# Kernel tuning notes

Hardware: AMD Instinct MI355X
Metric: run time of the kernel (lower is better)

Reference implementation:

```python
import jax, jax.numpy as jnp
import numpy as np

D_MODEL = 512
NUM_HEADS = 8
D_K = D_MODEL // NUM_HEADS


def setup_inputs() -> dict:
    key = jax.random.key(0)
    k0, k1, k2, k3, k4 = jax.random.split(key, 5)
    s = 1.0 / np.sqrt(D_MODEL)
    return {
        "x": jax.random.normal(k0, (2, 4096, D_MODEL), dtype=jnp.float32),
        "W_q": jax.random.normal(k1, (D_MODEL, D_MODEL), dtype=jnp.float32) * s,
        "W_k": jax.random.normal(k2, (D_MODEL, D_MODEL), dtype=jnp.float32) * s,
        "W_v": jax.random.normal(k3, (D_MODEL, D_MODEL), dtype=jnp.float32) * s,
        "W_o": jax.random.normal(k4, (D_MODEL, D_MODEL), dtype=jnp.float32) * s,
    }


def reference(x, W_q, W_k, W_v, W_o):
    B, S, _ = x.shape
    # project and split heads: (B, H, S, d_k)
    def split(t):
        return t.reshape(B, S, NUM_HEADS, D_K).transpose(0, 2, 1, 3)
    Q = split(x @ W_q)
    K = split(x @ W_k)
    V = split(x @ W_v)
    scale = jnp.sqrt(jnp.asarray(D_K, dtype=x.dtype))
    logits = jnp.einsum('bhqd,bhkd->bhqk', Q, K) / scale
    attn = jax.nn.softmax(logits, axis=-1)  # dropout is identity at inference
    out = jnp.einsum('bhqk,bhkd->bhqd', attn, V)
    concat = out.transpose(0, 2, 1, 3).reshape(B, S, D_MODEL)
    return concat @ W_o
```

## Files before the change

kernel.cpp:

```cpp
#include <hip/hip_runtime.h>
#include <hip/hip_bf16.h>


#define DMODEL 512
#define SEQ    4096
#define NTOK   8192
#define LDQK   1024

using f32x4 = __attribute__((ext_vector_type(4))) float;
using s16x8 = __attribute__((ext_vector_type(8))) short;
using u16x8 = __attribute__((ext_vector_type(8))) unsigned short;

static __device__ __forceinline__ unsigned short f2bf(float f) {
  union { float f; unsigned u; } v; v.f = f;
  unsigned r = v.u + 0x7fff + ((v.u >> 16) & 1);
  return (unsigned short)(r >> 16);
}

static __device__ __forceinline__ unsigned pack_bf2(float lo, float hi) {
  __hip_bfloat162 t = __float22bfloat162_rn(make_float2(lo, hi));
  union { __hip_bfloat162 b; unsigned u; } c; c.b = t; return c.u;
}

static __device__ __forceinline__ void gll16(const void* g, void* l) {
  __builtin_amdgcn_global_load_lds(
      (const __attribute__((address_space(1))) unsigned int*)g,
      (__attribute__((address_space(3))) unsigned int*)l, 16, 0, 0);
}

__global__ void prep_kernel(const float* __restrict__ x,
                            const float* __restrict__ Wq,
                            const float* __restrict__ Wk,
                            const float* __restrict__ Wv,
                            const float* __restrict__ Wo,
                            unsigned short* __restrict__ xb,
                            unsigned short* __restrict__ Wall, float c2) {
  __shared__ float T[64][65];
  const int bx = blockIdx.x;
  if (bx < 1024) {
    for (int i = bx * 256 + threadIdx.x; i < NTOK * DMODEL / 4; i += 262144) {
      float4 v = ((const float4*)x)[i];
      ushort4 o;
      o.x = f2bf(v.x); o.y = f2bf(v.y); o.z = f2bf(v.z); o.w = f2bf(v.w);
      ((ushort4*)xb)[i] = o;
    }
    return;
  }
  const int t = bx - 1024;
  const int y = t >> 6, sub = t & 63;
  const float* W = (y == 0) ? Wq : (y == 1) ? Wk : (y == 2) ? Wv : Wo;
  const float scale = (y == 0) ? c2 : 1.0f;
  const int tk = (sub & 7) * 64;
  const int tn = (sub >> 3) * 64;
  const int r  = threadIdx.x >> 2;
  const int cq = threadIdx.x & 3;
#pragma unroll
  for (int i = 0; i < 4; ++i) {
    int c = (cq + 4 * i) * 4;
    float4 v = *(const float4*)&W[(size_t)(tk + r) * 512 + tn + c];
    T[r][c + 0] = v.x * scale; T[r][c + 1] = v.y * scale;
    T[r][c + 2] = v.z * scale; T[r][c + 3] = v.w * scale;
  }
  __syncthreads();
  const int n  = threadIdx.x >> 2;
  const int k0 = (threadIdx.x & 3) * 16;
#pragma unroll
  for (int j4 = 0; j4 < 4; ++j4) {
    ushort4 o;
    o.x = f2bf(T[k0 + j4 * 4 + 0][n]);
    o.y = f2bf(T[k0 + j4 * 4 + 1][n]);
    o.z = f2bf(T[k0 + j4 * 4 + 2][n]);
    o.w = f2bf(T[k0 + j4 * 4 + 3][n]);
    *(ushort4*)&Wall[(size_t)y * 262144 + (size_t)(tn + n) * 512 + tk + k0 + j4 * 4] = o;
  }
}

__global__ __launch_bounds__(256, 3) void gemm_qkv(
    const unsigned short* __restrict__ xb,
    const unsigned short* __restrict__ Wall,
    unsigned short* __restrict__ QKb,
    unsigned short* __restrict__ Vtb)
{
  __shared__ unsigned short As[128 * 32];
  __shared__ unsigned short Bs[128 * 32];
  const int by = blockIdx.y;
  const bool vmode = (by >= 8);
  const unsigned short* A  = vmode ? (Wall + 2 * 262144) : xb;
  const unsigned short* Bt = vmode ? xb : Wall;
  const size_t bm = vmode ? (size_t)(by - 8) * 128 : (size_t)blockIdx.x * 128;
  const size_t bn = vmode ? (size_t)blockIdx.x * 128 : (size_t)by * 128;
  const int tid  = threadIdx.x;
  const int wave = tid >> 6, lane = tid & 63;
  const int q4 = lane >> 4, ln = lane & 15;
  const int wm = (wave >> 1) * 64, wn = (wave & 1) * 64;
  f32x4 acc[4][4] = {};
  const int srow = wave * 16 + (lane >> 2);
  const int scol = (lane & 3) * 8;

  const unsigned short* Ag  = A  + (bm + srow)      * 512 + scol;
  const unsigned short* Ag2 = A  + (bm + 64 + srow) * 512 + scol;
  const unsigned short* Bg  = Bt + (bn + srow)      * 512 + scol;
  const unsigned short* Bg2 = Bt + (bn + 64 + srow) * 512 + scol;
  unsigned short* Ad  = As + wave * 512;
  unsigned short* Ad2 = As + 2048 + wave * 512;
  unsigned short* Bd  = Bs + wave * 512;
  unsigned short* Bd2 = Bs + 2048 + wave * 512;

  for (int kt = 0; kt < 512; kt += 32) {
    __syncthreads();
    gll16(Ag + kt,  Ad);
    gll16(Ag2 + kt, Ad2);
    gll16(Bg + kt,  Bd);
    gll16(Bg2 + kt, Bd2);
    __syncthreads();
    s16x8 af[4], bfr[4];
#pragma unroll
    for (int i = 0; i < 4; i++)
      af[i] = *(const s16x8*)(As + (wm + i * 16 + ln) * 32 + q4 * 8);
#pragma unroll
    for (int i = 0; i < 4; i++)
      bfr[i] = *(const s16x8*)(Bs + (wn + i * 16 + ln) * 32 + q4 * 8);
#pragma unroll
    for (int mi = 0; mi < 4; mi++)
#pragma unroll
      for (int ni = 0; ni < 4; ni++)
        acc[mi][ni] = __builtin_amdgcn_mfma_f32_16x16x32_bf16(
            af[mi], bfr[ni], acc[mi][ni], 0, 0, 0);
  }
#pragma unroll
  for (int mi = 0; mi < 4; mi++)
#pragma unroll
    for (int r = 0; r < 4; ++r) {
      size_t row = bm + wm + mi * 16 + q4 * 4 + r;
#pragma unroll
      for (int ni = 0; ni < 4; ni++) {
        size_t col = bn + wn + ni * 16 + ln;
        unsigned short hv = f2bf(acc[mi][ni][r]);
        if (!vmode) {
          QKb[row * 1024 + col] = hv;
        } else {
          int b = (int)(col >> 12), s = (int)(col & 4095);
          int sp = (s & ~63) | (s & 32) | (((s >> 2) & 3) << 3) |
                   (((s >> 4) & 1) << 2) | (s & 3);
          Vtb[(size_t)b * 2097152 + row * 4096 + sp] = hv;
        }
      }
    }
}

__global__ __launch_bounds__(256, 2) void attn_kernel(
    const unsigned short* __restrict__ QK,
    const unsigned short* __restrict__ Vt,
    float* __restrict__ Opart,
    float* __restrict__ Lpart)
{
  const int qt = blockIdx.x, h = blockIdx.y, z = blockIdx.z;
  const int b = z >> 1, ck = z & 1;
  const int tid = threadIdx.x, wave = tid >> 6, lane = tid & 63;
  const int q4 = lane >> 4, ln = lane & 15;
  __shared__ unsigned short Ks[2][64 * 72];
  __shared__ unsigned short Vs[2][64 * 72];
  const size_t rowbase = (size_t)b * SEQ;
  const size_t qrow0   = (size_t)qt * 128 + wave * 32;
  const unsigned short* Kp  = QK + rowbase * LDQK + 512 + h * 64;
  const unsigned short* VTp = Vt + ((size_t)(b * 8 + h) * 64) * SEQ;

  s16x8 qf[2][2];
#pragma unroll
  for (int mf = 0; mf < 2; ++mf) {
    const unsigned short* q = QK + (rowbase + qrow0 + mf * 16 + ln) * LDQK + h * 64;
    qf[mf][0] = *(const s16x8*)(q + q4 * 8);
    qf[mf][1] = *(const s16x8*)(q + 32 + q4 * 8);
  }
  f32x4 o[2][4] = {};
  float lp[2] = {};

  const int srow = tid >> 2;
  const int scol = (tid & 3) * 16;

  const unsigned short* kgp = Kp  + (size_t)(ck * 2048 + srow) * LDQK + scol;
  const unsigned short* vgp = VTp + (size_t)srow * SEQ + ck * 2048 + scol;

  u16x8 kr  = *(const u16x8*)kgp;
  u16x8 kr2 = *(const u16x8*)(kgp + 8);
  u16x8 vr  = *(const u16x8*)vgp;
  u16x8 vr2 = *(const u16x8*)(vgp + 8);
  *(u16x8*)(Ks[0] + srow * 72 + scol)     = kr;
  *(u16x8*)(Ks[0] + srow * 72 + scol + 8) = kr2;
  *(u16x8*)(Vs[0] + srow * 72 + scol)     = vr;
  *(u16x8*)(Vs[0] + srow * 72 + scol + 8) = vr2;
  kgp += (size_t)64 * LDQK;  vgp += 64;
  kr  = *(const u16x8*)kgp;
  kr2 = *(const u16x8*)(kgp + 8);
  vr  = *(const u16x8*)vgp;
  vr2 = *(const u16x8*)(vgp + 8);
  __syncthreads();

  for (int t = 0; t < 32; ++t) {
    const int cur = t & 1;
    const unsigned short* Kc = Ks[cur];
    const unsigned short* Vc = Vs[cur];

    f32x4 s4[2][4] = {};
#pragma unroll
    for (int ni = 0; ni < 4; ni++) {
      const unsigned short* kb = Kc + (ni * 16 + ln) * 72 + q4 * 8;
      s16x8 kf0 = *(const s16x8*)kb;
      s16x8 kf1 = *(const s16x8*)(kb + 32);
#pragma unroll
      for (int mf = 0; mf < 2; ++mf) {
        s4[mf][ni] = __builtin_amdgcn_mfma_f32_16x16x32_bf16(kf0, qf[mf][0], s4[mf][ni], 0, 0, 0);
        s4[mf][ni] = __builtin_amdgcn_mfma_f32_16x16x32_bf16(kf1, qf[mf][1], s4[mf][ni], 0, 0, 0);
      }
    }
    s16x8 vf[2][4];
#pragma unroll
    for (int ks = 0; ks < 2; ++ks)
#pragma unroll
      for (int ni = 0; ni < 4; ni++)
        vf[ks][ni] = *(const s16x8*)(Vc + (ni * 16 + ln) * 72 + ks * 32 + q4 * 8);

    s16x8 pf[2][2];
#pragma unroll
    for (int mf = 0; mf < 2; ++mf) {
      float e[4][4];
      float ls = 0.f;
#pragma unroll
      for (int ni = 0; ni < 4; ni++)
#pragma unroll
        for (int r = 0; r < 4; ++r) {
          e[ni][r] = __builtin_amdgcn_exp2f(s4[mf][ni][r]);
          ls += e[ni][r];
        }
      lp[mf] += ls;
#pragma unroll
      for (int ks = 0; ks < 2; ++ks) {
        union { s16x8 v; unsigned u[4]; } pu;
        pu.u[0] = pack_bf2(e[2 * ks][0],     e[2 * ks][1]);
        pu.u[1] = pack_bf2(e[2 * ks][2],     e[2 * ks][3]);
        pu.u[2] = pack_bf2(e[2 * ks + 1][0], e[2 * ks + 1][1]);
        pu.u[3] = pack_bf2(e[2 * ks + 1][2], e[2 * ks + 1][3]);
        pf[mf][ks] = pu.v;
      }
    }
#pragma unroll
    for (int ks = 0; ks < 2; ++ks)
#pragma unroll
      for (int ni = 0; ni < 4; ni++)
#pragma unroll
        for (int mf = 0; mf < 2; ++mf)
          o[mf][ni] = __builtin_amdgcn_mfma_f32_16x16x32_bf16(pf[mf][ks], vf[ks][ni], o[mf][ni], 0, 0, 0);

    if (t + 1 < 32) {
      unsigned short* Kn = Ks[cur ^ 1];
      unsigned short* Vn = Vs[cur ^ 1];
      *(u16x8*)(Kn + srow * 72 + scol)     = kr;
      *(u16x8*)(Kn + srow * 72 + scol + 8) = kr2;
      *(u16x8*)(Vn + srow * 72 + scol)     = vr;
      *(u16x8*)(Vn + srow * 72 + scol + 8) = vr2;
      if (t + 2 < 32) {
        kgp += (size_t)64 * LDQK;  vgp += 64;
        kr  = *(const u16x8*)kgp;
        kr2 = *(const u16x8*)(kgp + 8);
        vr  = *(const u16x8*)vgp;
        vr2 = *(const u16x8*)(vgp + 8);
      }
    }
    __syncthreads();
  }
#pragma unroll
  for (int mf = 0; mf < 2; ++mf) {
    float l = lp[mf];
    l += __shfl_xor(l, 16, 64);
    l += __shfl_xor(l, 32, 64);
    if (q4 == 0)
      Lpart[(size_t)ck * 65536 + (size_t)(b * 8 + h) * 4096 + qrow0 + mf * 16 + ln] = l;
  }
  float* Opc = Opart + (size_t)ck * NTOK * DMODEL;
#pragma unroll
  for (int mf = 0; mf < 2; ++mf)
#pragma unroll
    for (int r = 0; r < 4; ++r) {
      size_t row = rowbase + qrow0 + mf * 16 + q4 * 4 + r;
#pragma unroll
      for (int ni = 0; ni < 4; ni++)
        Opc[row * DMODEL + h * 64 + ni * 16 + ln] = o[mf][ni][r];
    }
}

__global__ __launch_bounds__(256, 2) void gemm_out(
    const float* __restrict__ Opart,
    const float* __restrict__ Lpart,
    const unsigned short* __restrict__ Bt,
    float* __restrict__ C)
{
  __shared__ unsigned short As[128 * 32];
  __shared__ unsigned short Bs[64 * 32];
  const int tid  = threadIdx.x;
  const int wave = tid >> 6, lane = tid & 63;
  const int q4 = lane >> 4, ln = lane & 15;
  const size_t bm = (size_t)blockIdx.x * 128;
  const size_t bn = (size_t)blockIdx.y * 64;
  const int wm = (wave >> 1) * 64, wn = (wave & 1) * 32;
  f32x4 acc[4][2] = {};
  const int srow = wave * 16 + (lane >> 2);
  const int scol = (lane & 3) * 8;

  const size_t r0 = bm + srow, r1 = bm + 64 + srow;
  float invA[8], invB[8];
  {
    const size_t q0 = r0 & 4095, b0 = r0 >> 12;
    const size_t q1 = r1 & 4095, b1 = r1 >> 12;
#pragma unroll
    for (int hh = 0; hh < 8; ++hh) {
      invA[hh] = 1.0f / (Lpart[(b0 * 8 + hh) * 4096 + q0] +
                         Lpart[65536 + (b0 * 8 + hh) * 4096 + q0]);
      invB[hh] = 1.0f / (Lpart[(b1 * 8 + hh) * 4096 + q1] +
                         Lpart[65536 + (b1 * 8 + hh) * 4096 + q1]);
    }
  }
  const float* A0a = Opart + r0 * 512;
  const float* A0b = Opart + (size_t)NTOK * DMODEL + r0 * 512;
  const float* A1a = Opart + r1 * 512;
  const float* A1b = Opart + (size_t)NTOK * DMODEL + r1 * 512;
  const unsigned short* Bg = Bt + (bn + srow) * 512 + scol;
  unsigned short* Bd = Bs + wave * 512;

  for (int kt = 0; kt < 512; kt += 32) {
    __syncthreads();
    gll16(Bg + kt, Bd);
    const int c0 = kt + scol;
    const int hh = c0 >> 6;
    {
      f32x4 xa = *(const f32x4*)(A0a + c0),  xa2 = *(const f32x4*)(A0a + c0 + 4);
      f32x4 xb = *(const f32x4*)(A0b + c0),  xb2 = *(const f32x4*)(A0b + c0 + 4);
      float iv = invA[hh];
      union { u16x8 v; unsigned u[4]; } pu;
      pu.u[0] = pack_bf2((xa[0] + xb[0]) * iv, (xa[1] + xb[1]) * iv);
      pu.u[1] = pack_bf2((xa[2] + xb[2]) * iv, (xa[3] + xb[3]) * iv);
      pu.u[2] = pack_bf2((xa2[0] + xb2[0]) * iv, (xa2[1] + xb2[1]) * iv);
      pu.u[3] = pack_bf2((xa2[2] + xb2[2]) * iv, (xa2[3] + xb2[3]) * iv);
      *(u16x8*)(As + srow * 32 + scol) = pu.v;
    }
    {
      f32x4 xa = *(const f32x4*)(A1a + c0),  xa2 = *(const f32x4*)(A1a + c0 + 4);
      f32x4 xb = *(const f32x4*)(A1b + c0),  xb2 = *(const f32x4*)(A1b + c0 + 4);
      float iv = invB[hh];
      union { u16x8 v; unsigned u[4]; } pu;
      pu.u[0] = pack_bf2((xa[0] + xb[0]) * iv, (xa[1] + xb[1]) * iv);
      pu.u[1] = pack_bf2((xa[2] + xb[2]) * iv, (xa[3] + xb[3]) * iv);
      pu.u[2] = pack_bf2((xa2[0] + xb2[0]) * iv, (xa2[1] + xb2[1]) * iv);
      pu.u[3] = pack_bf2((xa2[2] + xb2[2]) * iv, (xa2[3] + xb2[3]) * iv);
      *(u16x8*)(As + (64 + srow) * 32 + scol) = pu.v;
    }
    __syncthreads();
    s16x8 af[4], bfr[2];
#pragma unroll
    for (int i = 0; i < 4; i++)
      af[i] = *(const s16x8*)(As + (wm + i * 16 + ln) * 32 + q4 * 8);
#pragma unroll
    for (int i = 0; i < 2; i++)
      bfr[i] = *(const s16x8*)(Bs + (wn + i * 16 + ln) * 32 + q4 * 8);
#pragma unroll
    for (int mi = 0; mi < 4; mi++)
#pragma unroll
      for (int ni = 0; ni < 2; ni++)
        acc[mi][ni] = __builtin_amdgcn_mfma_f32_16x16x32_bf16(
            af[mi], bfr[ni], acc[mi][ni], 0, 0, 0);
  }
#pragma unroll
  for (int mi = 0; mi < 4; mi++)
#pragma unroll
    for (int r = 0; r < 4; ++r) {
      size_t row = bm + wm + mi * 16 + q4 * 4 + r;
#pragma unroll
      for (int ni = 0; ni < 2; ni++)
        C[row * 512 + bn + wn + ni * 16 + ln] = acc[mi][ni][r];
    }
}

extern "C" void kernel_launch(void* const* d_in, const int* in_sizes, int n_in,
                              void* d_out, int out_size, void* d_ws, size_t ws_size,
                              hipStream_t stream) {
  const float* x  = (const float*)d_in[0];
  const float* Wq = (const float*)d_in[1];
  const float* Wk = (const float*)d_in[2];
  const float* Wv = (const float*)d_in[3];
  const float* Wo = (const float*)d_in[4];

  char* ws = (char*)d_ws;
  unsigned short* xb    = (unsigned short*)(ws);
  unsigned short* Wall  = (unsigned short*)(ws + 8388608);
  unsigned short* QKb   = (unsigned short*)(ws + 10485760);
  unsigned short* Vtb   = (unsigned short*)(ws + 27262976);
  float*          Opart = (float*)(ws + 35651584);
  float*          Lpart = (float*)(ws + 69206016);

  const float C2 = 0.125f * 1.44269504088896f;

  hipLaunchKernelGGL(prep_kernel, dim3(1280), dim3(256), 0, stream,
                     x, Wq, Wk, Wv, Wo, xb, Wall, C2);
  hipLaunchKernelGGL(gemm_qkv, dim3(64, 12), dim3(256), 0, stream,
                     xb, Wall, QKb, Vtb);
  hipLaunchKernelGGL(attn_kernel, dim3(32, 8, 4), dim3(256), 0, stream,
                     QKb, Vtb, Opart, Lpart);
  hipLaunchKernelGGL(gemm_out, dim3(64, 8), dim3(256), 0, stream,
                     Opart, Lpart, Wall + 3 * 262144, (float*)d_out);
}
```

Before: 199.5 us.

## Split partial-attention combine into separate kernel and feed bf16 to output GEMM

Adds a combine kernel that sums the two split-K attention partials, normalizes by the summed row sums, and writes a bf16 activation buffer once. The output GEMM then loads bf16 tiles directly with async global-to-LDS copies instead of re-reading and combining the fp32 partials for every column block. This removes redundant fp32 traffic and per-tile conversion work in the GEMM, at the cost of an extra launch and an 8MB intermediate round trip. Launch bounds on the GEMM are raised to allow more resident blocks.

```diff
diff --git a/kernel.cpp b/kernel.cpp
--- a/kernel.cpp
+++ b/kernel.cpp
@@ -288,9 +288,28 @@
     }
 }
 
-__global__ __launch_bounds__(256, 2) void gemm_out(
-    const float* __restrict__ Opart,
-    const float* __restrict__ Lpart,
+__global__ void combine_kernel(const float* __restrict__ Opart,
+                               const float* __restrict__ Lpart,
+                               unsigned short* __restrict__ Oc) {
+  int i = blockIdx.x * 256 + threadIdx.x;
+  int row = i >> 7;
+  int c4  = (i & 127) * 4;
+  int b = row >> 12, qrow = row & 4095, h = c4 >> 6;
+  float l = Lpart[(size_t)(b * 8 + h) * 4096 + qrow] +
+            Lpart[65536 + (size_t)(b * 8 + h) * 4096 + qrow];
+  float inv = 1.0f / l;
+  f32x4 a = *(const f32x4*)(Opart + (size_t)row * 512 + c4);
+  f32x4 c = *(const f32x4*)(Opart + (size_t)NTOK * DMODEL + (size_t)row * 512 + c4);
+  float r0 = (a[0] + c[0]) * inv, r1 = (a[1] + c[1]) * inv;
+  float r2 = (a[2] + c[2]) * inv, r3 = (a[3] + c[3]) * inv;
+  uint2 w;
+  w.x = pack_bf2(r0, r1);
+  w.y = pack_bf2(r2, r3);
+  *(uint2*)&Oc[(size_t)row * 512 + c4] = w;
+}
+
+__global__ __launch_bounds__(256, 3) void gemm_out(
+    const unsigned short* __restrict__ A,
     const unsigned short* __restrict__ Bt,
     float* __restrict__ C)
 {
@@ -306,53 +325,18 @@
   const int srow = wave * 16 + (lane >> 2);
   const int scol = (lane & 3) * 8;
 
-  const size_t r0 = bm + srow, r1 = bm + 64 + srow;
-  float invA[8], invB[8];
-  {
-    const size_t q0 = r0 & 4095, b0 = r0 >> 12;
-    const size_t q1 = r1 & 4095, b1 = r1 >> 12;
-#pragma unroll
-    for (int hh = 0; hh < 8; ++hh) {
-      invA[hh] = 1.0f / (Lpart[(b0 * 8 + hh) * 4096 + q0] +
-                         Lpart[65536 + (b0 * 8 + hh) * 4096 + q0]);
-      invB[hh] = 1.0f / (Lpart[(b1 * 8 + hh) * 4096 + q1] +
-                         Lpart[65536 + (b1 * 8 + hh) * 4096 + q1]);
-    }
-  }
-  const float* A0a = Opart + r0 * 512;
-  const float* A0b = Opart + (size_t)NTOK * DMODEL + r0 * 512;
-  const float* A1a = Opart + r1 * 512;
-  const float* A1b = Opart + (size_t)NTOK * DMODEL + r1 * 512;
-  const unsigned short* Bg = Bt + (bn + srow) * 512 + scol;
-  unsigned short* Bd = Bs + wave * 512;
+  const unsigned short* Ag  = A  + (bm + srow)      * 512 + scol;
+  const unsigned short* Ag2 = A  + (bm + 64 + srow) * 512 + scol;
+  const unsigned short* Bg  = Bt + (bn + srow)      * 512 + scol;
+  unsigned short* Ad  = As + wave * 512;
+  unsigned short* Ad2 = As + 2048 + wave * 512;
+  unsigned short* Bd  = Bs + wave * 512;
 
   for (int kt = 0; kt < 512; kt += 32) {
     __syncthreads();
-    gll16(Bg + kt, Bd);
-    const int c0 = kt + scol;
-    const int hh = c0 >> 6;
-    {
-      f32x4 xa = *(const f32x4*)(A0a + c0),  xa2 = *(const f32x4*)(A0a + c0 + 4);
-      f32x4 xb = *(const f32x4*)(A0b + c0),  xb2 = *(const f32x4*)(A0b + c0 + 4);
-      float iv = invA[hh];
-      union { u16x8 v; unsigned u[4]; } pu;
-      pu.u[0] = pack_bf2((xa[0] + xb[0]) * iv, (xa[1] + xb[1]) * iv);
-      pu.u[1] = pack_bf2((xa[2] + xb[2]) * iv, (xa[3] + xb[3]) * iv);
-      pu.u[2] = pack_bf2((xa2[0] + xb2[0]) * iv, (xa2[1] + xb2[1]) * iv);
-      pu.u[3] = pack_bf2((xa2[2] + xb2[2]) * iv, (xa2[3] + xb2[3]) * iv);
-      *(u16x8*)(As + srow * 32 + scol) = pu.v;
-    }
-    {
-      f32x4 xa = *(const f32x4*)(A1a + c0),  xa2 = *(const f32x4*)(A1a + c0 + 4);
-      f32x4 xb = *(const f32x4*)(A1b + c0),  xb2 = *(const f32x4*)(A1b + c0 + 4);
-      float iv = invB[hh];
-      union { u16x8 v; unsigned u[4]; } pu;
-      pu.u[0] = pack_bf2((xa[0] + xb[0]) * iv, (xa[1] + xb[1]) * iv);
-      pu.u[1] = pack_bf2((xa[2] + xb[2]) * iv, (xa[3] + xb[3]) * iv);
-      pu.u[2] = pack_bf2((xa2[0] + xb2[0]) * iv, (xa2[1] + xb2[1]) * iv);
-      pu.u[3] = pack_bf2((xa2[2] + xb2[2]) * iv, (xa2[3] + xb2[3]) * iv);
-      *(u16x8*)(As + (64 + srow) * 32 + scol) = pu.v;
-    }
+    gll16(Ag + kt,  Ad);
+    gll16(Ag2 + kt, Ad2);
+    gll16(Bg + kt,  Bd);
     __syncthreads();
     s16x8 af[4], bfr[2];
 #pragma unroll
@@ -393,8 +377,9 @@
   unsigned short* Wall  = (unsigned short*)(ws + 8388608);
   unsigned short* QKb   = (unsigned short*)(ws + 10485760);
   unsigned short* Vtb   = (unsigned short*)(ws + 27262976);
-  float*          Opart = (float*)(ws + 35651584);
-  float*          Lpart = (float*)(ws + 69206016);
+  unsigned short* Oc    = (unsigned short*)(ws + 35651584);
+  float*          Opart = (float*)(ws + 44040192);
+  float*          Lpart = (float*)(ws + 77594624);
 
   const float C2 = 0.125f * 1.44269504088896f;
 
@@ -404,6 +389,8 @@
                      xb, Wall, QKb, Vtb);
   hipLaunchKernelGGL(attn_kernel, dim3(32, 8, 4), dim3(256), 0, stream,
                      QKb, Vtb, Opart, Lpart);
+  hipLaunchKernelGGL(combine_kernel, dim3(4096), dim3(256), 0, stream,
+                     Opart, Lpart, Oc);
   hipLaunchKernelGGL(gemm_out, dim3(64, 8), dim3(256), 0, stream,
-                     Opart, Lpart, Wall + 3 * 262144, (float*)d_out);
-}
+                     Oc, Wall + 3 * 262144, (float*)d_out);
+}
```

After: 190.7 us. 1.05x faster.
